# Kernel optimization log

Hardware: AMD Instinct MI355X
Metric: run time of the kernel (lower is better)

The kernel has to match this reference:

```python
import jax, jax.numpy as jnp
import numpy as np

OBS = 256      # observation_space_size == state_vector_len
SV = 2047      # STATE_VECTORS = WMG_MAX_OBS
D = 256        # tfm_vec_size = 8 heads * 32 head_size
H = 8
HD = 32
L = 2          # TFM_NUM_LAYERS
FF = 1024      # TFM_HIDDEN_SIZE
ACH = 512      # AC_HIDDEN_LAYER_SIZE
A = 16         # action_space_size


def setup_inputs() -> dict:
    key = jax.random.key(0)
    ks = jax.random.split(key, 24)
    r = lambda k, s: (jax.random.normal(k, s, jnp.float32) * 0.02)
    inp = {
        "observation": jax.random.normal(ks[0], (OBS,), jnp.float32),
        "old_vectors": jax.random.normal(ks[1], (SV, OBS), jnp.float32),
        "W_core": r(ks[2], (OBS, D)), "b_core": jnp.zeros((D,), jnp.float32),
        # memo embedding takes cat(state_vec, age_onehot) of size OBS+SV
        "W_memo": r(ks[3], (OBS + SV, D)), "b_memo": jnp.zeros((D,), jnp.float32),
        "Wq": r(ks[4], (L, D, D)), "bq": jnp.zeros((L, D), jnp.float32),
        "Wk": r(ks[5], (L, D, D)), "bk": jnp.zeros((L, D), jnp.float32),
        "Wv": r(ks[6], (L, D, D)), "bv": jnp.zeros((L, D), jnp.float32),
        "Wo": r(ks[7], (L, D, D)), "bo": jnp.zeros((L, D), jnp.float32),
        "ln1_g": jnp.ones((L, D), jnp.float32), "ln1_b": jnp.zeros((L, D), jnp.float32),
        "ln2_g": jnp.ones((L, D), jnp.float32), "ln2_b": jnp.zeros((L, D), jnp.float32),
        "W_ff1": r(ks[8], (L, D, FF)), "b_ff1": jnp.zeros((L, FF), jnp.float32),
        "W_ff2": r(ks[9], (L, FF, D)), "b_ff2": jnp.zeros((L, D), jnp.float32),
        "aW1": r(ks[10], (D, ACH)), "ab1": jnp.zeros((ACH,), jnp.float32),
        "aW2": r(ks[11], (ACH, ACH)), "ab2": jnp.zeros((ACH,), jnp.float32),
        "aWo": r(ks[12], (ACH, A)), "abo": jnp.zeros((A,), jnp.float32),
        "cW1": r(ks[13], (D, ACH)), "cb1": jnp.zeros((ACH,), jnp.float32),
        "cW2": r(ks[14], (ACH, ACH)), "cb2": jnp.zeros((ACH,), jnp.float32),
        "cWo": r(ks[15], (ACH, 1)), "cbo": jnp.zeros((1,), jnp.float32),
    }
    return inp


def _ln(x, g, b, eps=1e-5):
    m = jnp.mean(x, axis=-1, keepdims=True)
    v = jnp.mean(jnp.square(x - m), axis=-1, keepdims=True)
    return (x - m) * jax.lax.rsqrt(v + eps) * g + b


def reference(observation, old_vectors, W_core, b_core, W_memo, b_memo,
              Wq, bq, Wk, bk, Wv, bv, Wo, bo,
              ln1_g, ln1_b, ln2_g, ln2_b, W_ff1, b_ff1, W_ff2, b_ff2,
              aW1, ab1, aW2, ab2, aWo, abo, cW1, cb1, cW2, cb2, cWo, cbo):
    # core embedding [D]
    emb0 = observation @ W_core + b_core
    # fused memo + age-onehot embedding: cat(vec_i, e_i) @ W_memo == vec_i @ W_memo[:OBS] + W_memo[OBS+i]
    memo_emb = old_vectors @ W_memo[:OBS] + W_memo[OBS:] + b_memo  # [SV, D]
    x = jnp.concatenate([emb0[None, :], memo_emb], axis=0)[None]   # [1, 1+SV, D]
    S = 1 + SV
    scale = 1.0 / np.sqrt(HD).astype(np.float32)
    for l in range(L):
        q = (x @ Wq[l] + bq[l]).reshape(1, S, H, HD)
        k = (x @ Wk[l] + bk[l]).reshape(1, S, H, HD)
        v = (x @ Wv[l] + bv[l]).reshape(1, S, H, HD)
        scores = jnp.einsum('bqhd,bkhd->bhqk', q, k) * scale       # [1,H,S,S]
        probs = jax.nn.softmax(scores, axis=-1)
        ctx = jnp.einsum('bhqk,bkhd->bqhd', probs, v).reshape(1, S, D)
        x = _ln(x + ctx @ Wo[l] + bo[l], ln1_g[l], ln1_b[l])
        h = jax.nn.gelu(x @ W_ff1[l] + b_ff1[l])
        x = _ln(x + h @ W_ff2[l] + b_ff2[l], ln2_g[l], ln2_b[l])
    t = x[:, 0, :]                                                 # [1, D]
    ha = jnp.tanh(jnp.tanh(t @ aW1 + ab1) @ aW2 + ab2)
    policy = ha @ aWo + abo                                        # [1, A] logits
    hc = jnp.tanh(jnp.tanh(t @ cW1 + cb1) @ cW2 + cb2)
    value_est = hc @ cWo + cbo                                     # [1, 1]
    # WMG_MAX_MEMOS == 0 path: new state vector is tanh(observation)
    new_vector = jnp.tanh(observation)                             # [OBS]
    return value_est, policy, new_vector
```

## Files before the change

kernel.cpp:

```cpp
#include <hip/hip_runtime.h>
#include <stdint.h>

typedef __attribute__((ext_vector_type(8))) short bf16x8;
typedef __attribute__((ext_vector_type(4))) float f32x4;

constexpr int kSEQ = 2048;
constexpr int kD   = 256;
constexpr int kHD  = 32;
constexpr int kFF  = 1024;
constexpr int kA   = 16;

__device__ __forceinline__ unsigned short f2b(float f) {
  union { float f; unsigned int u; } v; v.f = f;
  unsigned int r = v.u + 0x7FFFu + ((v.u >> 16) & 1u);
  return (unsigned short)(r >> 16);
}

struct ConvTable {
  const float* src[13];
  int K[13];
  int N[13];
  int dst[13];
  int tstart[14];
};

union SharedU {
  struct { unsigned short lt[64][72]; } cv;
  struct { unsigned short Al[64][40]; unsigned short Bl[32][40]; } g64;
  struct { unsigned short Kl[64][40]; unsigned short Vt[32][72];
           unsigned short Pl[4][16][72]; } at;
  struct { unsigned short As[16][264]; float2 red[4][16]; } lg;
};

struct MegaParams {
  ConvTable tab;
  const float *obs, *oldv, *Wcore, *bcore, *Wmemo0, *bmemo, *Wmemo2;
  const float *bq, *bk, *bv, *bo, *ln1g, *ln1b, *ln2g, *ln2b, *bff1, *bff2;
  const float *aW1, *ab1, *aW2, *ab2, *aWo, *abo;
  const float *cW1, *cb1, *cW2, *cb2, *cWo, *cbo;
  float* xf; unsigned short* xb;
  unsigned short *qb, *kb, *vb, *hb, *wT;
  float *pacc, *pml, *pf, *out;
  int oQKV[2], oWoT[2], oFF1[2], oFF2[2];
  int convJobs, nsplit, tpb;
};

__device__ void conv_job(const MegaParams& p, SharedU& sh, int job) {
  const int tid = threadIdx.x;
  if (job == p.convJobs) {
    float a = p.bcore[tid];
    #pragma unroll 8
    for (int k = 0; k < 256; k++) a += p.obs[k] * p.Wcore[k * kD + tid];
    p.xf[tid] = a;
    p.xb[tid] = f2b(a);
    return;
  }
  int m = 0;
  while (job >= p.tab.tstart[m + 1]) m++;
  const int tloc = job - p.tab.tstart[m];
  const int N = p.tab.N[m], K = p.tab.K[m];
  const int ntile = N >> 6;
  const int k0 = (tloc / ntile) * 64, n0 = (tloc % ntile) * 64;
  const float* src = p.tab.src[m];
  {
    const int r = tid >> 2, c16 = (tid & 3) * 16;
    const float* sp = src + (size_t)(k0 + r) * N + n0 + c16;
    #pragma unroll
    for (int j = 0; j < 16; j++) sh.cv.lt[r][c16 + j] = f2b(sp[j]);
  }
  __syncthreads();
  {
    const int n = tid >> 2, kc = (tid & 3) * 16;
    unsigned short* dp = p.wT + p.tab.dst[m] + (size_t)(n0 + n) * K + k0 + kc;
    unsigned short g[16];
    #pragma unroll
    for (int j = 0; j < 16; j++) g[j] = sh.cv.lt[kc + j][n];
    *(bf16x8*)dp = *(bf16x8*)&g[0];
    *(bf16x8*)(dp + 8) = *(bf16x8*)&g[8];
  }
}

__device__ void memo_job(const MegaParams& p, SharedU& sh, int job) {
  const int tid = threadIdx.x;
  const int w = tid >> 6, l = tid & 63, lg = l >> 4, lr = l & 15;
  const int sr = tid >> 2, sk = (tid & 3) * 8;
  const int kr = tid >> 3, nc = (tid & 7) * 4;
  const int m0 = (job & 31) * 64, n0 = (job >> 5) * 32;
  f32x4 acc[2];
  #pragma unroll
  for (int c = 0; c < 2; c++)
    #pragma unroll
    for (int i = 0; i < 4; i++) acc[c][i] = 0.f;

  auto loadA = [&](int k0) -> bf16x8 {
    bf16x8 av;
    if (m0 + sr < 2047) {
      const float* ap = p.oldv + (size_t)(m0 + sr) * 256 + k0 + sk;
      #pragma unroll
      for (int j = 0; j < 8; j++) av[j] = (short)f2b(ap[j]);
    } else {
      #pragma unroll
      for (int j = 0; j < 8; j++) av[j] = 0;
    }
    return av;
  };
  auto loadB = [&](int k0, float* b4) {
    const float* bp = p.Wmemo0 + (size_t)(k0 + kr) * kD + n0 + nc;
    #pragma unroll
    for (int j = 0; j < 4; j++) b4[j] = bp[j];
  };

  bf16x8 av = loadA(0);
  float b4[4];
  loadB(0, b4);

  for (int k0 = 0; k0 < 256; k0 += 32) {
    __syncthreads();
    *(bf16x8*)&sh.g64.Al[sr][sk] = av;
    #pragma unroll
    for (int j = 0; j < 4; j++) sh.g64.Bl[nc + j][kr] = f2b(b4[j]);
    __syncthreads();
    if (k0 + 32 < 256) {
      av = loadA(k0 + 32);
      loadB(k0 + 32, b4);
    }
    bf16x8 af = *(bf16x8*)&sh.g64.Al[w * 16 + lr][8 * lg];
    #pragma unroll
    for (int c = 0; c < 2; c++) {
      bf16x8 bf = *(bf16x8*)&sh.g64.Bl[c * 16 + lr][8 * lg];
      acc[c] = __builtin_amdgcn_mfma_f32_16x16x32_bf16(af, bf, acc[c], 0, 0, 0);
    }
  }

  #pragma unroll
  for (int c = 0; c < 2; c++)
    #pragma unroll
    for (int i = 0; i < 4; i++) {
      const int gr = m0 + w * 16 + 4 * lg + i;
      const int gc = n0 + c * 16 + lr;
      if (gr >= 2047) continue;
      const float v = acc[c][i] + p.bmemo[gc] + p.Wmemo2[(size_t)gr * kD + gc];
      p.xf[(size_t)(gr + 1) * kD + gc] = v;
      p.xb[(size_t)(gr + 1) * kD + gc] = f2b(v);
    }
}

__global__ __launch_bounds__(256) void k_cvm(MegaParams p) {
  __shared__ SharedU sh;
  if (blockIdx.x < 256) memo_job(p, sh, blockIdx.x);
  else conv_job(p, sh, blockIdx.x - 256);
}

template <int EPI>
__device__ __forceinline__ void gemm_job(
    SharedU& sh, int m0, int n0, const unsigned short* Ap, int lda, int Kloop,
    const unsigned short* BT, int ldb,
    const float* p0, const float* p1, const float* p2,
    void* o0, void* o1, void* o2) {
  const int tid = threadIdx.x;
  const int w = tid >> 6, l = tid & 63, lg = l >> 4, lr = l & 15;
  const int sr = tid >> 2, sk = (tid & 3) * 8;
  f32x4 acc[2];
  #pragma unroll
  for (int c = 0; c < 2; c++)
    #pragma unroll
    for (int i = 0; i < 4; i++) acc[c][i] = 0.f;

  bf16x8 av = *(const bf16x8*)(Ap + (size_t)(m0 + sr) * lda + sk);
  bf16x8 bv;
  if (tid < 128) bv = *(const bf16x8*)(BT + (size_t)(n0 + sr) * ldb + sk);

  for (int k0 = 0; k0 < Kloop; k0 += 32) {
    __syncthreads();
    *(bf16x8*)&sh.g64.Al[sr][sk] = av;
    if (tid < 128) *(bf16x8*)&sh.g64.Bl[sr][sk] = bv;
    __syncthreads();
    if (k0 + 32 < Kloop) {
      av = *(const bf16x8*)(Ap + (size_t)(m0 + sr) * lda + k0 + 32 + sk);
      if (tid < 128)
        bv = *(const bf16x8*)(BT + (size_t)(n0 + sr) * ldb + k0 + 32 + sk);
    }
    bf16x8 af = *(bf16x8*)&sh.g64.Al[w * 16 + lr][8 * lg];
    #pragma unroll
    for (int c = 0; c < 2; c++) {
      bf16x8 bf = *(bf16x8*)&sh.g64.Bl[c * 16 + lr][8 * lg];
      acc[c] = __builtin_amdgcn_mfma_f32_16x16x32_bf16(af, bf, acc[c], 0, 0, 0);
    }
  }

  #pragma unroll
  for (int c = 0; c < 2; c++) {
    #pragma unroll
    for (int i = 0; i < 4; i++) {
      const int gr = m0 + w * 16 + 4 * lg + i;
      const int gc = n0 + c * 16 + lr;
      float v = acc[c][i];
      if constexpr (EPI == 1) {
        const int t = gc >> 8, cc = gc & 255;
        const float* bp = (t == 0) ? p0 : (t == 1 ? p1 : p2);
        unsigned short* op = (t == 0) ? (unsigned short*)o0
                              : (t == 1 ? (unsigned short*)o1
                                        : (unsigned short*)o2);
        v += bp[cc];
        if (t == 0) v *= 0.17677669529663687f;
        op[(size_t)gr * kD + cc] = f2b(v);
      } else if constexpr (EPI == 2) {
        v += p0[gc];
        const float g =
            0.5f * v *
            (1.0f + tanhf(0.7978845608028654f * (v + 0.044715f * v * v * v)));
        ((unsigned short*)o0)[(size_t)gr * kFF + gc] = f2b(g);
      } else {
        ((float*)o0)[(size_t)gr * kD + gc] = v;
      }
    }
  }
}

__global__ __launch_bounds__(256) void k_qkv(MegaParams p, int lyr) {
  __shared__ SharedU sh;
  for (int job = blockIdx.x; job < 768; job += gridDim.x) {
    const int m0 = (job & 31) * 64, n0 = (job >> 5) * 32;
    gemm_job<1>(sh, m0, n0, p.xb, 256, 256, p.wT + p.oQKV[lyr], 256,
                p.bq + lyr * 256, p.bk + lyr * 256, p.bv + lyr * 256,
                p.qb, p.kb, p.vb);
  }
}

__global__ __launch_bounds__(256) void k_ff1(MegaParams p, int lyr) {
  __shared__ SharedU sh;
  for (int job = blockIdx.x; job < 1024; job += gridDim.x) {
    const int m0 = (job & 31) * 64, n0 = (job >> 5) * 32;
    gemm_job<2>(sh, m0, n0, p.xb, 256, 256, p.wT + p.oFF1[lyr], 256,
                p.bff1 + lyr * 1024, nullptr, nullptr, p.hb, nullptr, nullptr);
  }
}

__global__ __launch_bounds__(256) void k_ff2p(MegaParams p, int lyr) {
  __shared__ SharedU sh;
  for (int job = blockIdx.x; job < 1024; job += gridDim.x) {
    const int m0 = (job & 31) * 64;
    const int n0 = ((job >> 5) & 7) * 32;
    const int kc = (job >> 8) * 256;
    gemm_job<3>(sh, m0, n0, p.hb + kc, kFF, 256,
                p.wT + p.oFF2[lyr] + kc, kFF, nullptr, nullptr, nullptr,
                p.pf + (size_t)(job >> 8) * kSEQ * kD, nullptr, nullptr);
  }
}

__device__ void attn_job(SharedU& sh, int qb_, int h, int s, int tpb,
                         const unsigned short* q, const unsigned short* k,
                         const unsigned short* v, float* pacc, float* pml) {
  const int tid = threadIdx.x;
  const int w = tid >> 6, l = tid & 63, lg = l >> 4, lr = l & 15;
  const int q0 = qb_ * 64;
  const int hoff = h * kHD;
  const int sr = tid >> 2, sk = (tid & 3) * 8;
  const int t0 = s * tpb;

  const bf16x8 qf =
      *(const bf16x8*)(q + (size_t)(q0 + w * 16 + lr) * kD + hoff + 8 * lg);

  float m_[4], l_[4];
  f32x4 acc[2];
  #pragma unroll
  for (int i = 0; i < 4; i++) { m_[i] = -1e30f; l_[i] = 0.f; }
  #pragma unroll
  for (int dt = 0; dt < 2; dt++)
    #pragma unroll
    for (int i = 0; i < 4; i++) acc[dt][i] = 0.f;

  bf16x8 kreg = *(const bf16x8*)(k + (size_t)(t0 * 64 + sr) * kD + hoff + sk);
  bf16x8 vreg = *(const bf16x8*)(v + (size_t)(t0 * 64 + sr) * kD + hoff + sk);

  for (int t = 0; t < tpb; t++) {
    __syncthreads();
    *(bf16x8*)&sh.at.Kl[sr][sk] = kreg;
    #pragma unroll
    for (int j = 0; j < 8; j++) sh.at.Vt[sk + j][sr] = (unsigned short)vreg[j];
    __syncthreads();
    if (t + 1 < tpb) {
      const size_t nx = (size_t)((t0 + t + 1) * 64 + sr) * kD + hoff + sk;
      kreg = *(const bf16x8*)(k + nx);
      vreg = *(const bf16x8*)(v + nx);
    }
    f32x4 sc[4];
    #pragma unroll
    for (int c = 0; c < 4; c++) {
      f32x4 z;
      #pragma unroll
      for (int i = 0; i < 4; i++) z[i] = 0.f;
      bf16x8 kf = *(bf16x8*)&sh.at.Kl[c * 16 + lr][8 * lg];
      sc[c] = __builtin_amdgcn_mfma_f32_16x16x32_bf16(qf, kf, z, 0, 0, 0);
    }
    float tm[4];
    #pragma unroll
    for (int i = 0; i < 4; i++)
      tm[i] = fmaxf(fmaxf(sc[0][i], sc[1][i]), fmaxf(sc[2][i], sc[3][i]));
    #pragma unroll
    for (int mm = 1; mm <= 8; mm <<= 1)
      #pragma unroll
      for (int i = 0; i < 4; i++) tm[i] = fmaxf(tm[i], __shfl_xor(tm[i], mm));
    float pv[4][4], rs[4], corr[4];
    #pragma unroll
    for (int i = 0; i < 4; i++) {
      const float nm = fmaxf(m_[i], tm[i]);
      corr[i] = __expf(m_[i] - nm);
      m_[i] = nm;
      rs[i] = 0.f;
    }
    #pragma unroll
    for (int c = 0; c < 4; c++)
      #pragma unroll
      for (int i = 0; i < 4; i++) {
        pv[c][i] = __expf(sc[c][i] - m_[i]);
        rs[i] += pv[c][i];
      }
    #pragma unroll
    for (int mm = 1; mm <= 8; mm <<= 1)
      #pragma unroll
      for (int i = 0; i < 4; i++) rs[i] += __shfl_xor(rs[i], mm);
    #pragma unroll
    for (int i = 0; i < 4; i++) {
      l_[i] = l_[i] * corr[i] + rs[i];
      acc[0][i] *= corr[i];
      acc[1][i] *= corr[i];
    }
    #pragma unroll
    for (int c = 0; c < 4; c++)
      #pragma unroll
      for (int i = 0; i < 4; i++)
        sh.at.Pl[w][4 * lg + i][c * 16 + lr] = f2b(pv[c][i]);
    __syncthreads();
    #pragma unroll
    for (int k2 = 0; k2 < 2; k2++) {
      bf16x8 pf_ = *(bf16x8*)&sh.at.Pl[w][lr][k2 * 32 + 8 * lg];
      #pragma unroll
      for (int dt = 0; dt < 2; dt++) {
        bf16x8 vf = *(bf16x8*)&sh.at.Vt[dt * 16 + lr][k2 * 32 + 8 * lg];
        acc[dt] = __builtin_amdgcn_mfma_f32_16x16x32_bf16(pf_, vf, acc[dt], 0, 0, 0);
      }
    }
  }

  const int pb = s * 8 + h;
  float* pa = pacc + (size_t)pb * kSEQ * kHD;
  float* pm = pml + (size_t)pb * kSEQ * 2;
  #pragma unroll
  for (int dt = 0; dt < 2; dt++)
    #pragma unroll
    for (int i = 0; i < 4; i++) {
      const int gr = q0 + w * 16 + 4 * lg + i;
      pa[(size_t)gr * kHD + dt * 16 + lr] = acc[dt][i];
    }
  if (lr == 0) {
    #pragma unroll
    for (int i = 0; i < 4; i++) {
      const int gr = q0 + w * 16 + 4 * lg + i;
      float2 ml; ml.x = m_[i]; ml.y = l_[i];
      *(float2*)&pm[(size_t)gr * 2] = ml;
    }
  }
}

__global__ __launch_bounds__(256) void k_attn(MegaParams p) {
  __shared__ SharedU sh;
  const int njobs = 256 * p.nsplit;
  for (int job = blockIdx.x; job < njobs; job += gridDim.x) {
    const int qb_ = job & 31, h = (job >> 5) & 7, s = job >> 8;
    attn_job(sh, qb_, h, s, p.tpb, p.qb, p.kb, p.vb, p.pacc, p.pml);
  }
}

__device__ __forceinline__ void ln_write(SharedU& sh, float vloc[4][4], int r0,
                                         const float* gam, const float* bet,
                                         float* xf, unsigned short* xb) {
  const int tid = threadIdx.x;
  const int w = tid >> 6, l = tid & 63, lg = l >> 4, lr = l & 15;
  float ps[4], ps2[4];
  #pragma unroll
  for (int i = 0; i < 4; i++) {
    ps[i] = 0.f; ps2[i] = 0.f;
    #pragma unroll
    for (int c = 0; c < 4; c++) {
      ps[i] += vloc[c][i];
      ps2[i] += vloc[c][i] * vloc[c][i];
    }
  }
  #pragma unroll
  for (int mm = 1; mm <= 8; mm <<= 1)
    #pragma unroll
    for (int i = 0; i < 4; i++) {
      ps[i] += __shfl_xor(ps[i], mm);
      ps2[i] += __shfl_xor(ps2[i], mm);
    }
  if (lr == 0) {
    #pragma unroll
    for (int i = 0; i < 4; i++) {
      float2 t; t.x = ps[i]; t.y = ps2[i];
      sh.lg.red[w][4 * lg + i] = t;
    }
  }
  __syncthreads();
  #pragma unroll
  for (int i = 0; i < 4; i++) {
    const int ri = 4 * lg + i;
    float sx = 0.f, sx2 = 0.f;
    #pragma unroll
    for (int ww = 0; ww < 4; ww++) {
      float2 t = sh.lg.red[ww][ri];
      sx += t.x; sx2 += t.y;
    }
    const float mean = sx * (1.0f / 256.0f);
    const float var = sx2 * (1.0f / 256.0f) - mean * mean;
    const float rstd = rsqrtf(var + 1e-5f);
    const int gr = r0 + ri;
    #pragma unroll
    for (int c = 0; c < 4; c++) {
      const int col = w * 64 + c * 16 + lr;
      const float y = (vloc[c][i] - mean) * rstd * gam[col] + bet[col];
      xf[(size_t)gr * kD + col] = y;
      xb[(size_t)gr * kD + col] = f2b(y);
    }
  }
}

__global__ __launch_bounds__(256) void k_woln(MegaParams p, int lyr) {
  __shared__ SharedU sh;
  const unsigned short* BT = p.wT + p.oWoT[lyr];
  const float* bias = p.bo + lyr * kD;
  const float* gam = p.ln1g + lyr * kD;
  const float* bet = p.ln1b + lyr * kD;
  const int tid = threadIdx.x;
  const int w = tid >> 6, l = tid & 63, lg = l >> 4, lr = l & 15;
  for (int job = blockIdx.x; job < 128; job += gridDim.x) {
    const int r0 = job * 16;
    __syncthreads();
    {
      const int row = r0 + (tid >> 4);
      const int kc = (tid & 15) * 16;
      const int h_ = kc >> 5;
      float mx = -1e30f;
      for (int s2 = 0; s2 < p.nsplit; s2++)
        mx = fmaxf(mx, p.pml[((size_t)(s2 * 8 + h_) * kSEQ + row) * 2]);
      float L = 0.f;
      const int d0 = kc & 31;
      float o[16];
      #pragma unroll
      for (int j = 0; j < 16; j++) o[j] = 0.f;
      for (int s2 = 0; s2 < p.nsplit; s2++) {
        const size_t pb = (size_t)(s2 * 8 + h_) * kSEQ + row;
        const float2 t = *(const float2*)&p.pml[pb * 2];
        const float es = __expf(t.x - mx);
        L += t.y * es;
        const float* pa = p.pacc + pb * kHD + d0;
        #pragma unroll
        for (int j = 0; j < 16; j++) o[j] += pa[j] * es;
      }
      const float inv = 1.0f / L;
      unsigned short* dst = &sh.lg.As[tid >> 4][kc];
      #pragma unroll
      for (int j = 0; j < 16; j++) dst[j] = f2b(o[j] * inv);
    }
    __syncthreads();
    f32x4 acc[4];
    #pragma unroll
    for (int c = 0; c < 4; c++)
      #pragma unroll
      for (int i = 0; i < 4; i++) acc[c][i] = 0.f;
    #pragma unroll 2
    for (int k0 = 0; k0 < 256; k0 += 32) {
      bf16x8 af = *(bf16x8*)&sh.lg.As[lr][k0 + 8 * lg];
      #pragma unroll
      for (int c = 0; c < 4; c++) {
        bf16x8 bf = *(const bf16x8*)(BT + (size_t)(w * 64 + c * 16 + lr) * 256 +
                                     k0 + 8 * lg);
        acc[c] = __builtin_amdgcn_mfma_f32_16x16x32_bf16(af, bf, acc[c], 0, 0, 0);
      }
    }
    float vloc[4][4];
    #pragma unroll
    for (int c = 0; c < 4; c++)
      #pragma unroll
      for (int i = 0; i < 4; i++) {
        const int col = w * 64 + c * 16 + lr;
        const int gr = r0 + 4 * lg + i;
        vloc[c][i] = acc[c][i] + bias[col] + p.xf[(size_t)gr * kD + col];
      }
    ln_write(sh, vloc, r0, gam, bet, p.xf, p.xb);
  }
}

template <bool WH>
__global__ __launch_bounds__(256) void k_ln2r(MegaParams p, int lyr) {
  __shared__ float tl[256];
  __shared__ float hA[1024];
  __shared__ float hB[1024];
  __shared__ float vred[4];
  const float* bias = p.bff2 + lyr * kD;
  const float* gam = p.ln2g + lyr * kD;
  const float* bet = p.ln2b + lyr * kD;
  const int tid = threadIdx.x;
  const int w = tid >> 6, l = tid & 63;
  const int row = blockIdx.x * 4 + w;
  f32x4 v = *(const f32x4*)(p.xf + (size_t)row * kD + l * 4);
  f32x4 b4 = *(const f32x4*)(bias + l * 4);
  #pragma unroll
  for (int i = 0; i < 4; i++) v[i] += b4[i];
  #pragma unroll
  for (int s = 0; s < 4; s++) {
    f32x4 t = *(const f32x4*)(p.pf + ((size_t)s * kSEQ + row) * kD + l * 4);
    #pragma unroll
    for (int i = 0; i < 4; i++) v[i] += t[i];
  }
  float su = v[0] + v[1] + v[2] + v[3];
  #pragma unroll
  for (int mm = 1; mm < 64; mm <<= 1) su += __shfl_xor(su, mm);
  const float mn = su * (1.0f / 256.0f);
  const float d0 = v[0] - mn, d1 = v[1] - mn, d2 = v[2] - mn, d3 = v[3] - mn;
  float s2 = d0 * d0 + d1 * d1 + d2 * d2 + d3 * d3;
  #pragma unroll
  for (int mm = 1; mm < 64; mm <<= 1) s2 += __shfl_xor(s2, mm);
  const float rstd = rsqrtf(s2 * (1.0f / 256.0f) + 1e-5f);
  f32x4 g4 = *(const f32x4*)(gam + l * 4);
  f32x4 be4 = *(const f32x4*)(bet + l * 4);
  f32x4 y;
  y[0] = d0 * rstd * g4[0] + be4[0];
  y[1] = d1 * rstd * g4[1] + be4[1];
  y[2] = d2 * rstd * g4[2] + be4[2];
  y[3] = d3 * rstd * g4[3] + be4[3];
  *(f32x4*)(p.xf + (size_t)row * kD + l * 4) = y;
  unsigned long long pk = (unsigned long long)f2b(y[0]) |
                          ((unsigned long long)f2b(y[1]) << 16) |
                          ((unsigned long long)f2b(y[2]) << 32) |
                          ((unsigned long long)f2b(y[3]) << 48);
  *(unsigned long long*)(p.xb + (size_t)row * kD + l * 4) = pk;

  if constexpr (WH) {
    if (blockIdx.x == 0) {
      if (w == 0) *(f32x4*)&tl[l * 4] = y;
      __syncthreads();
      float a0 = p.ab1[tid], a1 = p.ab1[tid + 256];
      float c0 = p.cb1[tid], c1 = p.cb1[tid + 256];
      for (int k = 0; k < 256; k++) {
        const float x = tl[k];
        a0 += x * p.aW1[(size_t)k * 512 + tid];
        a1 += x * p.aW1[(size_t)k * 512 + tid + 256];
        c0 += x * p.cW1[(size_t)k * 512 + tid];
        c1 += x * p.cW1[(size_t)k * 512 + tid + 256];
      }
      hA[tid] = tanhf(a0); hA[tid + 256] = tanhf(a1);
      hA[512 + tid] = tanhf(c0); hA[768 + tid] = tanhf(c1);
      __syncthreads();
      float b0 = p.ab2[tid], b1 = p.ab2[tid + 256];
      float e0 = p.cb2[tid], e1 = p.cb2[tid + 256];
      for (int k = 0; k < 512; k++) {
        const float xa = hA[k], xc = hA[512 + k];
        b0 += xa * p.aW2[(size_t)k * 512 + tid];
        b1 += xa * p.aW2[(size_t)k * 512 + tid + 256];
        e0 += xc * p.cW2[(size_t)k * 512 + tid];
        e1 += xc * p.cW2[(size_t)k * 512 + tid + 256];
      }
      hB[tid] = tanhf(b0); hB[tid + 256] = tanhf(b1);
      hB[512 + tid] = tanhf(e0); hB[768 + tid] = tanhf(e1);
      __syncthreads();
      const int g = tid >> 4, l16 = tid & 15;
      float s = 0.f;
      for (int k2 = l16 * 32; k2 < l16 * 32 + 32; k2++)
        s += hB[k2] * p.aWo[(size_t)k2 * kA + g];
      #pragma unroll
      for (int mm = 1; mm <= 8; mm <<= 1) s += __shfl_xor(s, mm);
      if (l16 == 0) p.out[1 + g] = s + p.abo[g];
      float vv = hB[512 + tid] * p.cWo[tid] + hB[768 + tid] * p.cWo[tid + 256];
      #pragma unroll
      for (int mm = 1; mm <= 32; mm <<= 1) vv += __shfl_xor(vv, mm);
      if ((tid & 63) == 0) vred[tid >> 6] = vv;
      __syncthreads();
      if (tid == 0)
        p.out[0] = vred[0] + vred[1] + vred[2] + vred[3] + p.cbo[0];
      p.out[17 + tid] = tanhf(p.obs[tid]);
    }
  }
}

extern "C" void kernel_launch(void* const* d_in, const int* in_sizes, int n_in,
                              void* d_out, int out_size, void* d_ws, size_t ws_size,
                              hipStream_t stream) {
  const float* obs   = (const float*)d_in[0];
  const float* oldv  = (const float*)d_in[1];
  const float* Wcore = (const float*)d_in[2];
  const float* bcore = (const float*)d_in[3];
  const float* Wmemo = (const float*)d_in[4];
  const float* bmemo = (const float*)d_in[5];
  const float* Wq    = (const float*)d_in[6];
  const float* bq    = (const float*)d_in[7];
  const float* Wk    = (const float*)d_in[8];
  const float* bk    = (const float*)d_in[9];
  const float* Wv    = (const float*)d_in[10];
  const float* bv    = (const float*)d_in[11];
  const float* Wo    = (const float*)d_in[12];
  const float* bo    = (const float*)d_in[13];
  const float* ln1g  = (const float*)d_in[14];
  const float* ln1b  = (const float*)d_in[15];
  const float* ln2g  = (const float*)d_in[16];
  const float* ln2b  = (const float*)d_in[17];
  const float* Wff1  = (const float*)d_in[18];
  const float* bff1  = (const float*)d_in[19];
  const float* Wff2  = (const float*)d_in[20];
  const float* bff2  = (const float*)d_in[21];

  MegaParams P;
  P.obs = obs; P.oldv = oldv; P.Wcore = Wcore; P.bcore = bcore;
  P.Wmemo0 = Wmemo; P.bmemo = bmemo; P.Wmemo2 = Wmemo + 256 * 256;
  P.bq = bq; P.bk = bk; P.bv = bv; P.bo = bo;
  P.ln1g = ln1g; P.ln1b = ln1b; P.ln2g = ln2g; P.ln2b = ln2b;
  P.bff1 = bff1; P.bff2 = bff2;
  P.aW1 = (const float*)d_in[22]; P.ab1 = (const float*)d_in[23];
  P.aW2 = (const float*)d_in[24]; P.ab2 = (const float*)d_in[25];
  P.aWo = (const float*)d_in[26]; P.abo = (const float*)d_in[27];
  P.cW1 = (const float*)d_in[28]; P.cb1 = (const float*)d_in[29];
  P.cW2 = (const float*)d_in[30]; P.cb2 = (const float*)d_in[31];
  P.cWo = (const float*)d_in[32]; P.cbo = (const float*)d_in[33];

  char* ws = (char*)d_ws;
  P.xf = (float*)(ws + 0);
  P.xb = (unsigned short*)(ws + (2u << 20));
  P.qb = (unsigned short*)(ws + (3u << 20));
  P.kb = (unsigned short*)(ws + (4u << 20));
  P.vb = (unsigned short*)(ws + (5u << 20));
  P.hb = (unsigned short*)(ws + (6u << 20));
  P.wT = (unsigned short*)(ws + (10u << 20));
  P.out = (float*)d_out;

  int nsplit = 8;
  const size_t paccOff = (size_t)14u << 20;
  const size_t pmlOff  = (size_t)31u << 20;
  const size_t pfOff   = (size_t)33u << 20;
  while (nsplit > 1 &&
         (paccOff + (size_t)nsplit * 8 * kSEQ * kHD * 4 > pmlOff ||
          pfOff + (size_t)4 * kSEQ * kD * 4 > ws_size))
    nsplit >>= 1;
  P.pacc = (float*)(ws + paccOff);
  P.pml  = (float*)(ws + pmlOff);
  P.pf   = (float*)(ws + pfOff);
  P.nsplit = nsplit;
  P.tpb = 32 / nsplit;

  int cur = 0;
  for (int l2 = 0; l2 < 2; l2++) {
    P.oQKV[l2] = cur; cur += 196608;
    P.oWoT[l2] = cur; cur += 65536;
    P.oFF1[l2] = cur; cur += 262144;
    P.oFF2[l2] = cur; cur += 262144;
  }

  int idx = 0, ts = 0;
  auto add = [&](const float* s, int K, int N, int dst) {
    P.tab.src[idx] = s; P.tab.K[idx] = K; P.tab.N[idx] = N;
    P.tab.dst[idx] = dst; P.tab.tstart[idx] = ts;
    ts += (K >> 6) * (N >> 6); idx++;
  };
  for (int l2 = 0; l2 < 2; l2++) {
    add(Wq + l2 * 65536, 256, 256, P.oQKV[l2]);
    add(Wk + l2 * 65536, 256, 256, P.oQKV[l2] + 65536);
    add(Wv + l2 * 65536, 256, 256, P.oQKV[l2] + 131072);
    add(Wo + l2 * 65536, 256, 256, P.oWoT[l2]);
    add(Wff1 + l2 * 262144, 256, 1024, P.oFF1[l2]);
    add(Wff2 + l2 * 262144, 1024, 256, P.oFF2[l2]);
  }
  P.tab.tstart[idx] = ts;
  P.convJobs = ts;

  k_cvm<<<256 + ts + 1, 256, 0, stream>>>(P);
  for (int lyr = 0; lyr < 2; lyr++) {
    k_qkv<<<768, 256, 0, stream>>>(P, lyr);
    k_attn<<<256 * nsplit, 256, 0, stream>>>(P);
    k_woln<<<128, 256, 0, stream>>>(P, lyr);
    k_ff1<<<1024, 256, 0, stream>>>(P, lyr);
    k_ff2p<<<1024, 256, 0, stream>>>(P, lyr);
    if (lyr == 0) k_ln2r<false><<<512, 256, 0, stream>>>(P, lyr);
    else          k_ln2r<true><<<512, 256, 0, stream>>>(P, lyr);
  }
}
```

Measured before the change: 236.5 us.

## Split serial actor-critic head into parallel multi-block kernels, drop grid-stride loops

The actor/critic MLP head used to run on a single block at the end of the last LN2 kernel, which serialises roughly a million weight reads on one CU. It now runs as three kernels: two 16-block GEMV stages that split output columns and reduce over K in shared memory, then a final small reduction kernel. The change also replaces grid-stride loops with one job per block in the GEMM and attention kernels, and rewrites the GELU tanh as an exp-based sigmoid form. The cost is two extra kernel launches and a small workspace area for the intermediate activations.

```diff
diff --git a/kernel.cpp b/kernel.cpp
--- a/kernel.cpp
+++ b/kernel.cpp
@@ -40,7 +40,7 @@
   const float *cW1, *cb1, *cW2, *cb2, *cWo, *cbo;
   float* xf; unsigned short* xb;
   unsigned short *qb, *kb, *vb, *hb, *wT;
-  float *pacc, *pml, *pf, *out;
+  float *pacc, *pml, *pf, *h1, *h2, *out;
   int oQKV[2], oWoT[2], oFF1[2], oFF2[2];
   int convJobs, nsplit, tpb;
 };
@@ -206,9 +206,8 @@
         op[(size_t)gr * kD + cc] = f2b(v);
       } else if constexpr (EPI == 2) {
         v += p0[gc];
-        const float g =
-            0.5f * v *
-            (1.0f + tanhf(0.7978845608028654f * (v + 0.044715f * v * v * v)));
+        const float u = 0.7978845608028654f * (v + 0.044715f * v * v * v);
+        const float g = v / (1.0f + __expf(-2.0f * u));
         ((unsigned short*)o0)[(size_t)gr * kFF + gc] = f2b(g);
       } else {
         ((float*)o0)[(size_t)gr * kD + gc] = v;
@@ -219,33 +218,30 @@
 
 __global__ __launch_bounds__(256) void k_qkv(MegaParams p, int lyr) {
   __shared__ SharedU sh;
-  for (int job = blockIdx.x; job < 768; job += gridDim.x) {
-    const int m0 = (job & 31) * 64, n0 = (job >> 5) * 32;
-    gemm_job<1>(sh, m0, n0, p.xb, 256, 256, p.wT + p.oQKV[lyr], 256,
-                p.bq + lyr * 256, p.bk + lyr * 256, p.bv + lyr * 256,
-                p.qb, p.kb, p.vb);
-  }
+  const int job = blockIdx.x;
+  const int m0 = (job & 31) * 64, n0 = (job >> 5) * 32;
+  gemm_job<1>(sh, m0, n0, p.xb, 256, 256, p.wT + p.oQKV[lyr], 256,
+              p.bq + lyr * 256, p.bk + lyr * 256, p.bv + lyr * 256,
+              p.qb, p.kb, p.vb);
 }
 
 __global__ __launch_bounds__(256) void k_ff1(MegaParams p, int lyr) {
   __shared__ SharedU sh;
-  for (int job = blockIdx.x; job < 1024; job += gridDim.x) {
-    const int m0 = (job & 31) * 64, n0 = (job >> 5) * 32;
-    gemm_job<2>(sh, m0, n0, p.xb, 256, 256, p.wT + p.oFF1[lyr], 256,
-                p.bff1 + lyr * 1024, nullptr, nullptr, p.hb, nullptr, nullptr);
-  }
+  const int job = blockIdx.x;
+  const int m0 = (job & 31) * 64, n0 = (job >> 5) * 32;
+  gemm_job<2>(sh, m0, n0, p.xb, 256, 256, p.wT + p.oFF1[lyr], 256,
+              p.bff1 + lyr * 1024, nullptr, nullptr, p.hb, nullptr, nullptr);
 }
 
 __global__ __launch_bounds__(256) void k_ff2p(MegaParams p, int lyr) {
   __shared__ SharedU sh;
-  for (int job = blockIdx.x; job < 1024; job += gridDim.x) {
-    const int m0 = (job & 31) * 64;
-    const int n0 = ((job >> 5) & 7) * 32;
-    const int kc = (job >> 8) * 256;
-    gemm_job<3>(sh, m0, n0, p.hb + kc, kFF, 256,
-                p.wT + p.oFF2[lyr] + kc, kFF, nullptr, nullptr, nullptr,
-                p.pf + (size_t)(job >> 8) * kSEQ * kD, nullptr, nullptr);
-  }
+  const int job = blockIdx.x;
+  const int m0 = (job & 31) * 64;
+  const int n0 = ((job >> 5) & 7) * 32;
+  const int kc = (job >> 8) * 256;
+  gemm_job<3>(sh, m0, n0, p.hb + kc, kFF, 256,
+              p.wT + p.oFF2[lyr] + kc, kFF, nullptr, nullptr, nullptr,
+              p.pf + (size_t)(job >> 8) * kSEQ * kD, nullptr, nullptr);
 }
 
 __device__ void attn_job(SharedU& sh, int qb_, int h, int s, int tpb,
@@ -365,11 +361,9 @@
 
 __global__ __launch_bounds__(256) void k_attn(MegaParams p) {
   __shared__ SharedU sh;
-  const int njobs = 256 * p.nsplit;
-  for (int job = blockIdx.x; job < njobs; job += gridDim.x) {
-    const int qb_ = job & 31, h = (job >> 5) & 7, s = job >> 8;
-    attn_job(sh, qb_, h, s, p.tpb, p.qb, p.kb, p.vb, p.pacc, p.pml);
-  }
+  const int job = blockIdx.x;
+  const int qb_ = job & 31, h = (job >> 5) & 7, s = job >> 8;
+  attn_job(sh, qb_, h, s, p.tpb, p.qb, p.kb, p.vb, p.pacc, p.pml);
 }
 
 __device__ __forceinline__ void ln_write(SharedU& sh, float vloc[4][4], int r0,
@@ -433,75 +427,66 @@
   const float* bet = p.ln1b + lyr * kD;
   const int tid = threadIdx.x;
   const int w = tid >> 6, l = tid & 63, lg = l >> 4, lr = l & 15;
-  for (int job = blockIdx.x; job < 128; job += gridDim.x) {
-    const int r0 = job * 16;
-    __syncthreads();
-    {
-      const int row = r0 + (tid >> 4);
-      const int kc = (tid & 15) * 16;
-      const int h_ = kc >> 5;
-      float mx = -1e30f;
-      for (int s2 = 0; s2 < p.nsplit; s2++)
-        mx = fmaxf(mx, p.pml[((size_t)(s2 * 8 + h_) * kSEQ + row) * 2]);
-      float L = 0.f;
-      const int d0 = kc & 31;
-      float o[16];
-      #pragma unroll
-      for (int j = 0; j < 16; j++) o[j] = 0.f;
-      for (int s2 = 0; s2 < p.nsplit; s2++) {
-        const size_t pb = (size_t)(s2 * 8 + h_) * kSEQ + row;
-        const float2 t = *(const float2*)&p.pml[pb * 2];
-        const float es = __expf(t.x - mx);
-        L += t.y * es;
-        const float* pa = p.pacc + pb * kHD + d0;
-        #pragma unroll
-        for (int j = 0; j < 16; j++) o[j] += pa[j] * es;
-      }
-      const float inv = 1.0f / L;
-      unsigned short* dst = &sh.lg.As[tid >> 4][kc];
-      #pragma unroll
-      for (int j = 0; j < 16; j++) dst[j] = f2b(o[j] * inv);
-    }
-    __syncthreads();
-    f32x4 acc[4];
-    #pragma unroll
-    for (int c = 0; c < 4; c++)
-      #pragma unroll
-      for (int i = 0; i < 4; i++) acc[c][i] = 0.f;
-    #pragma unroll 2
-    for (int k0 = 0; k0 < 256; k0 += 32) {
-      bf16x8 af = *(bf16x8*)&sh.lg.As[lr][k0 + 8 * lg];
-      #pragma unroll
-      for (int c = 0; c < 4; c++) {
-        bf16x8 bf = *(const bf16x8*)(BT + (size_t)(w * 64 + c * 16 + lr) * 256 +
-                                     k0 + 8 * lg);
-        acc[c] = __builtin_amdgcn_mfma_f32_16x16x32_bf16(af, bf, acc[c], 0, 0, 0);
-      }
-    }
-    float vloc[4][4];
-    #pragma unroll
-    for (int c = 0; c < 4; c++)
-      #pragma unroll
-      for (int i = 0; i < 4; i++) {
-        const int col = w * 64 + c * 16 + lr;
-        const int gr = r0 + 4 * lg + i;
-        vloc[c][i] = acc[c][i] + bias[col] + p.xf[(size_t)gr * kD + col];
-      }
-    ln_write(sh, vloc, r0, gam, bet, p.xf, p.xb);
-  }
-}
-
-template <bool WH>
+  const int r0 = blockIdx.x * 16;
+  {
+    const int row = r0 + (tid >> 4);
+    const int kc = (tid & 15) * 16;
+    const int h_ = kc >> 5;
+    float mx = -1e30f;
+    for (int s2 = 0; s2 < p.nsplit; s2++)
+      mx = fmaxf(mx, p.pml[((size_t)(s2 * 8 + h_) * kSEQ + row) * 2]);
+    float L = 0.f;
+    const int d0 = kc & 31;
+    float o[16];
+    #pragma unroll
+    for (int j = 0; j < 16; j++) o[j] = 0.f;
+    for (int s2 = 0; s2 < p.nsplit; s2++) {
+      const size_t pb = (size_t)(s2 * 8 + h_) * kSEQ + row;
+      const float2 t = *(const float2*)&p.pml[pb * 2];
+      const float es = __expf(t.x - mx);
+      L += t.y * es;
+      const float* pa = p.pacc + pb * kHD + d0;
+      #pragma unroll
+      for (int j = 0; j < 16; j++) o[j] += pa[j] * es;
+    }
+    const float inv = 1.0f / L;
+    unsigned short* dst = &sh.lg.As[tid >> 4][kc];
+    #pragma unroll
+    for (int j = 0; j < 16; j++) dst[j] = f2b(o[j] * inv);
+  }
+  __syncthreads();
+  f32x4 acc[4];
+  #pragma unroll
+  for (int c = 0; c < 4; c++)
+    #pragma unroll
+    for (int i = 0; i < 4; i++) acc[c][i] = 0.f;
+  #pragma unroll 2
+  for (int k0 = 0; k0 < 256; k0 += 32) {
+    bf16x8 af = *(bf16x8*)&sh.lg.As[lr][k0 + 8 * lg];
+    #pragma unroll
+    for (int c = 0; c < 4; c++) {
+      bf16x8 bf = *(const bf16x8*)(BT + (size_t)(w * 64 + c * 16 + lr) * 256 +
+                                   k0 + 8 * lg);
+      acc[c] = __builtin_amdgcn_mfma_f32_16x16x32_bf16(af, bf, acc[c], 0, 0, 0);
+    }
+  }
+  float vloc[4][4];
+  #pragma unroll
+  for (int c = 0; c < 4; c++)
+    #pragma unroll
+    for (int i = 0; i < 4; i++) {
+      const int col = w * 64 + c * 16 + lr;
+      const int gr = r0 + 4 * lg + i;
+      vloc[c][i] = acc[c][i] + bias[col] + p.xf[(size_t)gr * kD + col];
+    }
+  ln_write(sh, vloc, r0, gam, bet, p.xf, p.xb);
+}
+
 __global__ __launch_bounds__(256) void k_ln2r(MegaParams p, int lyr) {
-  __shared__ float tl[256];
-  __shared__ float hA[1024];
-  __shared__ float hB[1024];
-  __shared__ float vred[4];
   const float* bias = p.bff2 + lyr * kD;
   const float* gam = p.ln2g + lyr * kD;
   const float* bet = p.ln2b + lyr * kD;
-  const int tid = threadIdx.x;
-  const int w = tid >> 6, l = tid & 63;
+  const int w = threadIdx.x >> 6, l = threadIdx.x & 63;
   const int row = blockIdx.x * 4 + w;
   f32x4 v = *(const f32x4*)(p.xf + (size_t)row * kD + l * 4);
   f32x4 b4 = *(const f32x4*)(bias + l * 4);
@@ -535,52 +520,81 @@
                           ((unsigned long long)f2b(y[2]) << 32) |
                           ((unsigned long long)f2b(y[3]) << 48);
   *(unsigned long long*)(p.xb + (size_t)row * kD + l * 4) = pk;
-
-  if constexpr (WH) {
-    if (blockIdx.x == 0) {
-      if (w == 0) *(f32x4*)&tl[l * 4] = y;
-      __syncthreads();
-      float a0 = p.ab1[tid], a1 = p.ab1[tid + 256];
-      float c0 = p.cb1[tid], c1 = p.cb1[tid + 256];
-      for (int k = 0; k < 256; k++) {
-        const float x = tl[k];
-        a0 += x * p.aW1[(size_t)k * 512 + tid];
-        a1 += x * p.aW1[(size_t)k * 512 + tid + 256];
-        c0 += x * p.cW1[(size_t)k * 512 + tid];
-        c1 += x * p.cW1[(size_t)k * 512 + tid + 256];
-      }
-      hA[tid] = tanhf(a0); hA[tid + 256] = tanhf(a1);
-      hA[512 + tid] = tanhf(c0); hA[768 + tid] = tanhf(c1);
-      __syncthreads();
-      float b0 = p.ab2[tid], b1 = p.ab2[tid + 256];
-      float e0 = p.cb2[tid], e1 = p.cb2[tid + 256];
-      for (int k = 0; k < 512; k++) {
-        const float xa = hA[k], xc = hA[512 + k];
-        b0 += xa * p.aW2[(size_t)k * 512 + tid];
-        b1 += xa * p.aW2[(size_t)k * 512 + tid + 256];
-        e0 += xc * p.cW2[(size_t)k * 512 + tid];
-        e1 += xc * p.cW2[(size_t)k * 512 + tid + 256];
-      }
-      hB[tid] = tanhf(b0); hB[tid + 256] = tanhf(b1);
-      hB[512 + tid] = tanhf(e0); hB[768 + tid] = tanhf(e1);
-      __syncthreads();
-      const int g = tid >> 4, l16 = tid & 15;
-      float s = 0.f;
-      for (int k2 = l16 * 32; k2 < l16 * 32 + 32; k2++)
-        s += hB[k2] * p.aWo[(size_t)k2 * kA + g];
-      #pragma unroll
-      for (int mm = 1; mm <= 8; mm <<= 1) s += __shfl_xor(s, mm);
-      if (l16 == 0) p.out[1 + g] = s + p.abo[g];
-      float vv = hB[512 + tid] * p.cWo[tid] + hB[768 + tid] * p.cWo[tid + 256];
-      #pragma unroll
-      for (int mm = 1; mm <= 32; mm <<= 1) vv += __shfl_xor(vv, mm);
-      if ((tid & 63) == 0) vred[tid >> 6] = vv;
-      __syncthreads();
-      if (tid == 0)
-        p.out[0] = vred[0] + vred[1] + vred[2] + vred[3] + p.cbo[0];
-      p.out[17 + tid] = tanhf(p.obs[tid]);
-    }
-  }
+}
+
+__global__ __launch_bounds__(256) void k_h1(MegaParams p) {
+  __shared__ float tl[256];
+  __shared__ float red[4][64];
+  const int tid = threadIdx.x;
+  tl[tid] = p.xf[tid];
+  __syncthreads();
+  const int jj = blockIdx.x * 64;
+  const bool actor = jj < 512;
+  const float* W = actor ? p.aW1 : p.cW1;
+  const float* b = actor ? p.ab1 : p.cb1;
+  const int j0 = actor ? jj : jj - 512;
+  const int ks = tid >> 6, j = tid & 63;
+  float s = 0.f;
+  #pragma unroll 4
+  for (int k2 = ks * 64; k2 < ks * 64 + 64; k2++)
+    s += tl[k2] * W[(size_t)k2 * 512 + j0 + j];
+  red[ks][j] = s;
+  __syncthreads();
+  if (tid < 64) {
+    float t = red[0][tid] + red[1][tid] + red[2][tid] + red[3][tid] + b[j0 + tid];
+    p.h1[jj + tid] = tanhf(t);
+  }
+}
+
+__global__ __launch_bounds__(256) void k_h2(MegaParams p) {
+  __shared__ float tl[512];
+  __shared__ float red[4][64];
+  const int tid = threadIdx.x;
+  const int jj = blockIdx.x * 64;
+  const bool actor = jj < 512;
+  const float* hin = actor ? p.h1 : p.h1 + 512;
+  tl[tid] = hin[tid];
+  tl[tid + 256] = hin[tid + 256];
+  __syncthreads();
+  const float* W = actor ? p.aW2 : p.cW2;
+  const float* b = actor ? p.ab2 : p.cb2;
+  const int j0 = actor ? jj : jj - 512;
+  const int ks = tid >> 6, j = tid & 63;
+  float s = 0.f;
+  #pragma unroll 4
+  for (int k2 = ks * 128; k2 < ks * 128 + 128; k2++)
+    s += tl[k2] * W[(size_t)k2 * 512 + j0 + j];
+  red[ks][j] = s;
+  __syncthreads();
+  if (tid < 64) {
+    float t = red[0][tid] + red[1][tid] + red[2][tid] + red[3][tid] + b[j0 + tid];
+    p.h2[jj + tid] = tanhf(t);
+  }
+}
+
+__global__ __launch_bounds__(256) void k_h3(MegaParams p) {
+  __shared__ float ha[512], hc[512], vred[4];
+  const int tid = threadIdx.x;
+  ha[tid] = p.h2[tid];
+  ha[tid + 256] = p.h2[tid + 256];
+  hc[tid] = p.h2[512 + tid];
+  hc[tid + 256] = p.h2[768 + tid];
+  __syncthreads();
+  const int g = tid >> 4, l16 = tid & 15;
+  float s = 0.f;
+  for (int k2 = l16 * 32; k2 < l16 * 32 + 32; k2++)
+    s += ha[k2] * p.aWo[(size_t)k2 * kA + g];
+  #pragma unroll
+  for (int mm = 1; mm <= 8; mm <<= 1) s += __shfl_xor(s, mm);
+  if (l16 == 0) p.out[1 + g] = s + p.abo[g];
+  float vv = hc[tid] * p.cWo[tid] + hc[tid + 256] * p.cWo[tid + 256];
+  #pragma unroll
+  for (int mm = 1; mm <= 32; mm <<= 1) vv += __shfl_xor(vv, mm);
+  if ((tid & 63) == 0) vred[tid >> 6] = vv;
+  __syncthreads();
+  if (tid == 0)
+    p.out[0] = vred[0] + vred[1] + vred[2] + vred[3] + p.cbo[0];
+  p.out[17 + tid] = tanhf(p.obs[tid]);
 }
 
 extern "C" void kernel_launch(void* const* d_in, const int* in_sizes, int n_in,
@@ -638,11 +652,13 @@
   const size_t pfOff   = (size_t)33u << 20;
   while (nsplit > 1 &&
          (paccOff + (size_t)nsplit * 8 * kSEQ * kHD * 4 > pmlOff ||
-          pfOff + (size_t)4 * kSEQ * kD * 4 > ws_size))
+          pfOff + (size_t)4 * kSEQ * kD * 4 + 16384 > ws_size))
     nsplit >>= 1;
   P.pacc = (float*)(ws + paccOff);
   P.pml  = (float*)(ws + pmlOff);
   P.pf   = (float*)(ws + pfOff);
+  P.h1 = (float*)(ws + pfOff + (size_t)4 * kSEQ * kD * 4);
+  P.h2 = P.h1 + 1024;
   P.nsplit = nsplit;
   P.tpb = 32 / nsplit;
 
@@ -678,7 +694,9 @@
     k_woln<<<128, 256, 0, stream>>>(P, lyr);
     k_ff1<<<1024, 256, 0, stream>>>(P, lyr);
     k_ff2p<<<1024, 256, 0, stream>>>(P, lyr);
-    if (lyr == 0) k_ln2r<false><<<512, 256, 0, stream>>>(P, lyr);
-    else          k_ln2r<true><<<512, 256, 0, stream>>>(P, lyr);
-  }
-}
+    k_ln2r<<<512, 256, 0, stream>>>(P, lyr);
+  }
+  k_h1<<<16, 256, 0, stream>>>(P);
+  k_h2<<<16, 256, 0, stream>>>(P);
+  k_h3<<<1, 256, 0, stream>>>(P);
+}
```

After: 190.3 us. -19.5%, faster.
